# Kernel optimization log

Measured on AMD Instinct MI355X. Metric: run time of the kernel, lower is better.

The kernel has to match this reference:

```python
import jax, jax.numpy as jnp
import numpy as np

DIM = 512; LAYERS = 6; K = 15; VOCAB = 32000; B = 2; L = 1024
HID = 1024  # SwiGLU hidden: int(512*2) rounded up to multiple of 64
RANK = 64; BLOCK = 2048; MIX_W = 0.1
UP_DIL = [1, 2, 4, 8, 16, 32]
DN_DIL = UP_DIL[::-1]


def rmsnorm(x, w, eps=1e-6):
    return x * jax.lax.rsqrt(jnp.mean(x * x, axis=-1, keepdims=True) + eps) * w


def dconv(x, w, b, dil):
    # x: [B,D,T]; w: [D,1,K] depthwise; left (causal) padding of (K-1)*dil
    pad = (w.shape[-1] - 1) * dil
    y = jax.lax.conv_general_dilated(
        x, w, window_strides=(1,), padding=[(pad, 0)], rhs_dilation=(dil,),
        dimension_numbers=('NCH', 'OIH', 'NCH'), feature_group_count=x.shape[1])
    return y + b[None, :, None]


def conv_block(x, nw, cw, cb, w1, w2, w3, dil):
    # CausalDilatedConv: RMSNorm -> depthwise causal dilated conv -> silu -> SwiGLU -> +residual
    h = rmsnorm(x, nw)
    h = jax.nn.silu(dconv(jnp.transpose(h, (0, 2, 1)), cw, cb, dil))
    h = jnp.transpose(h, (0, 2, 1))
    h = jnp.einsum('bth,dh->btd',
                   jax.nn.silu(jnp.einsum('btd,hd->bth', h, w1)) * jnp.einsum('btd,hd->bth', h, w3),
                   w2)
    return h + x


def run_stack(x, dils, nw, cw, cb, w1, w2, w3, kp, ki, kd, gnorm):
    integral = x; previous = x; current = x
    for i, d in enumerate(dils):
        if i > 0:
            # PIDGate: step == i >= 1 so max(step,1) == i
            pid = kp[i-1] * current + ki[i-1] * (integral / i) + kd[i-1] * (current - previous)
            cur_in = rmsnorm(jax.nn.silu(pid), gnorm[i-1])
        else:
            cur_in = current
        current = conv_block(cur_in, nw[i], cw[i], cb[i], w1[i], w2[i], w3[i], d)
        previous = current
        integral = integral + current
    return current


def mix(x):
    # CausalMeanPool: x + 0.1 * causal running mean
    counts = jnp.arange(1, x.shape[1] + 1, dtype=x.dtype)[None, :, None]
    return x + MIX_W * jnp.cumsum(x, axis=1) / counts


def sgate(new, old, nw, dw, db, uw, ub):
    h = jax.nn.silu(rmsnorm(new, nw) @ dw.T + db)
    g = jax.nn.sigmoid(h @ uw.T + ub)
    return g * new + (1.0 - g) * old


def setup_inputs() -> dict:
    key = jax.random.key(0)
    ks = iter(jax.random.split(key, 64))
    def nrm(shape, s=0.02):
        return jax.random.normal(next(ks), shape, jnp.float32) * s
    def stack_params(p):
        return {
            p + '_norm_w': jnp.ones((LAYERS, DIM), jnp.float32),
            p + '_conv_w': nrm((LAYERS, DIM, 1, K), 0.1),
            p + '_conv_b': jnp.zeros((LAYERS, DIM), jnp.float32),
            p + '_w1': nrm((LAYERS, HID, DIM)),
            p + '_w2': nrm((LAYERS, DIM, HID)),
            p + '_w3': nrm((LAYERS, HID, DIM)),
            p + '_kp': jnp.full((LAYERS - 1, DIM), 0.5, jnp.float32),
            p + '_ki': jnp.full((LAYERS - 1, DIM), 0.3, jnp.float32),
            p + '_kd': jnp.full((LAYERS - 1, DIM), 0.2, jnp.float32),
            p + '_gnorm': jnp.ones((LAYERS - 1, DIM), jnp.float32),
        }
    inp = {
        'idx': jax.random.randint(next(ks), (B, L), 0, VOCAB),
        'emb': nrm((VOCAB, DIM)),
        'pos': nrm((1, BLOCK, DIM)),
        'emb_norm_w': jnp.ones((DIM,), jnp.float32),
        'token_shift': jnp.full((DIM,), 0.5, jnp.float32),
        'mem_gate_w': jnp.zeros((DIM, DIM), jnp.float32),  # nn.init.zeros_
        'mem_gate_b': nrm((DIM,)),
        'memory_p': jnp.zeros((B, DIM), jnp.float32),  # buffer, zero after reset()
        'sg_norm': jnp.ones((3, DIM), jnp.float32),
        'sg_down_w': nrm((3, RANK, DIM)),
        'sg_down_b': jnp.zeros((3, RANK), jnp.float32),
        'sg_up_w': nrm((3, DIM, RANK)),
        'sg_up_b': jnp.zeros((3, DIM), jnp.float32),
        'final_norm_w': jnp.ones((DIM,), jnp.float32),
    }
    inp.update(stack_params('up'))
    inp.update(stack_params('dn'))
    return inp


def _forward(idx, emb, pos, emb_norm_w, token_shift, mem_gate_w, mem_gate_b, memory_p,
             up_norm_w, up_conv_w, up_conv_b, up_w1, up_w2, up_w3, up_kp, up_ki, up_kd, up_gnorm,
             dn_norm_w, dn_conv_w, dn_conv_b, dn_w1, dn_w2, dn_w3, dn_kp, dn_ki, dn_kd, dn_gnorm,
             sg_norm, sg_down_w, sg_down_b, sg_up_w, sg_up_b, final_norm_w):
    T = idx.shape[1]
    x = emb[idx] + pos[:, :T]
    x = rmsnorm(x, emb_norm_w)
    # dropout is identity at eval time
    # memory injection: token-shift mix + sigmoid-gated persistent P-memory
    shifted = jnp.concatenate(
        [x[:, :1], token_shift * x[:, :-1] + (1.0 - token_shift) * x[:, 1:]], axis=1)
    mem = jax.nn.sigmoid(memory_p @ mem_gate_w.T + mem_gate_b)
    x = shifted + mem[:, None, :]
    initial = x
    up_p = (up_norm_w, up_conv_w, up_conv_b, up_w1, up_w2, up_w3, up_kp, up_ki, up_kd, up_gnorm)
    dn_p = (dn_norm_w, dn_conv_w, dn_conv_b, dn_w1, dn_w2, dn_w3, dn_kp, dn_ki, dn_kd, dn_gnorm)
    up1 = mix(run_stack(x, UP_DIL, *up_p))
    gated1 = sgate(up1, initial, sg_norm[0], sg_down_w[0], sg_down_b[0], sg_up_w[0], sg_up_b[0])
    down = mix(run_stack(gated1, DN_DIL, *dn_p))
    gated2 = sgate(down, initial, sg_norm[1], sg_down_w[1], sg_down_b[1], sg_up_w[1], sg_up_b[1])
    up2 = mix(run_stack(gated2, UP_DIL, *up_p))  # up_stack weights are shared/reused
    output = sgate(up2, gated2, sg_norm[2], sg_down_w[2], sg_down_b[2], sg_up_w[2], sg_up_b[2])
    output = rmsnorm(output, final_norm_w)
    return output @ emb.T  # tied head


def reference(idx, emb, pos, emb_norm_w, token_shift, mem_gate_w, mem_gate_b, memory_p,
              up_norm_w, up_conv_w, up_conv_b, up_w1, up_w2, up_w3, up_kp, up_ki, up_kd, up_gnorm,
              dn_norm_w, dn_conv_w, dn_conv_b, dn_w1, dn_w2, dn_w3, dn_kp, dn_ki, dn_kd, dn_gnorm,
              sg_norm, sg_down_w, sg_down_b, sg_up_w, sg_up_b, final_norm_w):
    return _forward(idx, emb, pos, emb_norm_w, token_shift, mem_gate_w, mem_gate_b, memory_p,
                    up_norm_w, up_conv_w, up_conv_b, up_w1, up_w2, up_w3, up_kp, up_ki, up_kd, up_gnorm,
                    dn_norm_w, dn_conv_w, dn_conv_b, dn_w1, dn_w2, dn_w3, dn_kp, dn_ki, dn_kd, dn_gnorm,
                    sg_norm, sg_down_w, sg_down_b, sg_up_w, sg_up_b, final_norm_w)
```

## Files before the change

kernel.cpp:

```cpp
#include <hip/hip_runtime.h>
#include <math.h>

#define DIM 512
#define NLAYERS 6
#define KSZ 15
#define VOCAB 32000
#define BATCH 2
#define SEQ 1024
#define HIDN 1024
#define RANK 64
#define NTOK (BATCH*SEQ)
#define MIXW 0.1f

typedef unsigned short u16;
typedef _Float16 f16;
typedef _Float16 f16x8 __attribute__((ext_vector_type(8)));
typedef _Float16 f16x4 __attribute__((ext_vector_type(4)));
typedef float  f32x4  __attribute__((ext_vector_type(4)));

__device__ __forceinline__ float sigm(float x){ return 1.f/(1.f+__expf(-x)); }

__device__ __forceinline__ float wred(float v){
  #pragma unroll
  for (int o=32;o>0;o>>=1) v += __shfl_xor(v, o, 64);
  return v;
}

#define MFMA16(a,b,c) __builtin_amdgcn_mfma_f32_16x16x32_f16(a,b,c,0,0,0)

__device__ __forceinline__ void gld16(const f16* g, f16* l){
  __builtin_amdgcn_global_load_lds(
      (const __attribute__((address_space(1))) void*)g,
      (__attribute__((address_space(3))) void*)l, 16, 0, 0);
}

template<int N> __device__ __forceinline__ void vwait(){
  asm volatile("s_waitcnt vmcnt(%0)" :: "i"(N) : "memory");
}
__device__ __forceinline__ void pipe_bar(){
  __builtin_amdgcn_s_barrier();
  __builtin_amdgcn_sched_barrier(0);
}

__global__ __launch_bounds__(256) void k_cvt(const float* __restrict__ s,
    f16* __restrict__ d, long n4){
  long i = (long)blockIdx.x*256 + threadIdx.x;
  if (i >= n4) return;
  float4 v = reinterpret_cast<const float4*>(s)[i];
  f16x4 o; o.x=(f16)v.x; o.y=(f16)v.y; o.z=(f16)v.z; o.w=(f16)v.w;
  reinterpret_cast<f16x4*>(d)[i] = o;
}

__global__ __launch_bounds__(256) void k_cvtconv(const float* __restrict__ cw,
    float* __restrict__ cwT, int n){
  int i = blockIdx.x*256 + threadIdx.x;
  if (i >= n) return;
  int d = i & (DIM-1); int m = (i >> 9) % KSZ; int l = i / (KSZ*DIM);
  cwT[i] = cw[((size_t)l*DIM + d)*KSZ + (KSZ-1-m)];
}

__global__ __launch_bounds__(64) void k_embnorm(const int* __restrict__ idx,
    const float* __restrict__ emb, const float* __restrict__ pos,
    const float* __restrict__ w, float* __restrict__ out){
  int row = blockIdx.x;
  int t = row & (SEQ-1);
  int lane = threadIdx.x;
  long ebase = (long)idx[row]*DIM;
  long pbase = (long)t*DIM;
  float v[8]; float ss = 0.f;
  #pragma unroll
  for (int c=0;c<2;c++){
    int d = c*256 + lane*4;
    float4 e = *reinterpret_cast<const float4*>(emb + ebase + d);
    float4 p = *reinterpret_cast<const float4*>(pos + pbase + d);
    float x0 = e.x+p.x, x1 = e.y+p.y, x2 = e.z+p.z, x3 = e.w+p.w;
    v[c*4+0]=x0; v[c*4+1]=x1; v[c*4+2]=x2; v[c*4+3]=x3;
    ss += x0*x0 + x1*x1 + x2*x2 + x3*x3;
  }
  ss = wred(ss);
  float rs = rsqrtf(ss*(1.f/DIM) + 1e-6f);
  long ob = (long)row*DIM;
  #pragma unroll
  for (int c=0;c<2;c++){
    int d = c*256 + lane*4;
    float4 wv = *reinterpret_cast<const float4*>(w + d);
    float4 o;
    o.x = v[c*4+0]*rs*wv.x; o.y = v[c*4+1]*rs*wv.y;
    o.z = v[c*4+2]*rs*wv.z; o.w = v[c*4+3]*rs*wv.w;
    *reinterpret_cast<float4*>(out + ob + d) = o;
  }
}

__global__ void k_mem(const float* __restrict__ p, const float* __restrict__ gw,
                      const float* __restrict__ gb, float* __restrict__ mem){
  int i = blockIdx.x*blockDim.x + threadIdx.x;
  if (i >= BATCH*DIM) return;
  int b = i >> 9, d = i & (DIM-1);
  float acc = gb[d];
  const float* wr = gw + (long)d*DIM;
  const float* pr = p + b*DIM;
  for (int k=0;k<DIM;k+=4){
    float4 wv = *reinterpret_cast<const float4*>(wr+k);
    float4 pv = *reinterpret_cast<const float4*>(pr+k);
    acc += wv.x*pv.x + wv.y*pv.y + wv.z*pv.z + wv.w*pv.w;
  }
  mem[i] = sigm(acc);
}

__global__ void k_shift(const float* __restrict__ xn, const float* __restrict__ mem,
    const float* __restrict__ ts, float* __restrict__ out){
  int i = blockIdx.x*256 + threadIdx.x;
  int d = i & (DIM-1); int row = i >> 9; int t = row & (SEQ-1); int b = row >> 10;
  float cur = xn[i];
  float v;
  if (t == 0) v = cur;
  else { float f = ts[d]; v = f*xn[i-DIM] + (1.f-f)*cur; }
  out[i] = v + mem[b*DIM + d];
}

__global__ __launch_bounds__(64) void k_rms(const float* __restrict__ x,
    const float* __restrict__ w, f16* __restrict__ oh){
  int row = blockIdx.x; int lane = threadIdx.x;
  const float* xr = x + (long)row*DIM;
  float v[8]; float ss = 0.f;
  #pragma unroll
  for (int c=0;c<2;c++){
    int d = c*256 + lane*4;
    float4 f = *reinterpret_cast<const float4*>(xr + d);
    v[c*4+0]=f.x; v[c*4+1]=f.y; v[c*4+2]=f.z; v[c*4+3]=f.w;
    ss += f.x*f.x + f.y*f.y + f.z*f.z + f.w*f.w;
  }
  ss = wred(ss);
  float rs = rsqrtf(ss*(1.f/DIM) + 1e-6f);
  long ob = (long)row*DIM;
  #pragma unroll
  for (int c=0;c<2;c++){
    int d = c*256 + lane*4;
    float4 wv = *reinterpret_cast<const float4*>(w + d);
    f16x4 o;
    o.x = (f16)(v[c*4+0]*rs*wv.x); o.y = (f16)(v[c*4+1]*rs*wv.y);
    o.z = (f16)(v[c*4+2]*rs*wv.z); o.w = (f16)(v[c*4+3]*rs*wv.w);
    *reinterpret_cast<f16x4*>(oh + ob + d) = o;
  }
}

__global__ __launch_bounds__(64) void k_pid(const float* __restrict__ C,
    const float* __restrict__ I, float inv_i,
    const float* __restrict__ kp, const float* __restrict__ ki,
    const float* __restrict__ gn, const float* __restrict__ nw,
    float* __restrict__ xin, f16* __restrict__ oh){
  int row = blockIdx.x; int lane = threadIdx.x;
  long base = (long)row*DIM;
  float u[8]; float ss = 0.f;
  #pragma unroll
  for (int c=0;c<2;c++){
    int d = c*256 + lane*4;
    float4 cv = *reinterpret_cast<const float4*>(C + base + d);
    float4 iv = *reinterpret_cast<const float4*>(I + base + d);
    float4 kpv = *reinterpret_cast<const float4*>(kp + d);
    float4 kiv = *reinterpret_cast<const float4*>(ki + d);
    float p0 = kpv.x*cv.x + kiv.x*(iv.x*inv_i);
    float p1 = kpv.y*cv.y + kiv.y*(iv.y*inv_i);
    float p2 = kpv.z*cv.z + kiv.z*(iv.z*inv_i);
    float p3 = kpv.w*cv.w + kiv.w*(iv.w*inv_i);
    float s0 = p0*sigm(p0), s1 = p1*sigm(p1), s2 = p2*sigm(p2), s3 = p3*sigm(p3);
    u[c*4+0]=s0; u[c*4+1]=s1; u[c*4+2]=s2; u[c*4+3]=s3;
    ss += s0*s0 + s1*s1 + s2*s2 + s3*s3;
  }
  ss = wred(ss);
  float rs1 = rsqrtf(ss*(1.f/DIM) + 1e-6f);
  float x2[8]; float ss2 = 0.f;
  #pragma unroll
  for (int c=0;c<2;c++){
    int d = c*256 + lane*4;
    float4 gv = *reinterpret_cast<const float4*>(gn + d);
    float y0 = u[c*4+0]*rs1*gv.x, y1 = u[c*4+1]*rs1*gv.y;
    float y2 = u[c*4+2]*rs1*gv.z, y3 = u[c*4+3]*rs1*gv.w;
    x2[c*4+0]=y0; x2[c*4+1]=y1; x2[c*4+2]=y2; x2[c*4+3]=y3;
    ss2 += y0*y0 + y1*y1 + y2*y2 + y3*y3;
    float4 o; o.x=y0; o.y=y1; o.z=y2; o.w=y3;
    *reinterpret_cast<float4*>(xin + base + d) = o;
  }
  ss2 = wred(ss2);
  float rs2 = rsqrtf(ss2*(1.f/DIM) + 1e-6f);
  #pragma unroll
  for (int c=0;c<2;c++){
    int d = c*256 + lane*4;
    float4 nv = *reinterpret_cast<const float4*>(nw + d);
    f16x4 o;
    o.x = (f16)(x2[c*4+0]*rs2*nv.x); o.y = (f16)(x2[c*4+1]*rs2*nv.y);
    o.z = (f16)(x2[c*4+2]*rs2*nv.z); o.w = (f16)(x2[c*4+3]*rs2*nv.w);
    *reinterpret_cast<f16x4*>(oh + base + d) = o;
  }
}

__global__ __launch_bounds__(256) void k_conv(const f16* __restrict__ h1,
    const float* __restrict__ cwT, const float* __restrict__ cb,
    f16* __restrict__ hc, int dil){
  int i = blockIdx.x*256 + threadIdx.x;
  int d8 = (i & 63) << 3; int row = i >> 6; int t = row & (SEQ-1);
  float acc[8];
  {
    float4 b0 = *reinterpret_cast<const float4*>(&cb[d8]);
    float4 b1 = *reinterpret_cast<const float4*>(&cb[d8+4]);
    acc[0]=b0.x; acc[1]=b0.y; acc[2]=b0.z; acc[3]=b0.w;
    acc[4]=b1.x; acc[5]=b1.y; acc[6]=b1.z; acc[7]=b1.w;
  }
  #pragma unroll
  for (int m=0;m<KSZ;m++){
    if (t - m*dil >= 0){
      f16x8 h = *reinterpret_cast<const f16x8*>(&h1[(size_t)(row - m*dil)*DIM + d8]);
      float4 w0 = *reinterpret_cast<const float4*>(&cwT[m*DIM + d8]);
      float4 w1 = *reinterpret_cast<const float4*>(&cwT[m*DIM + d8 + 4]);
      acc[0]+=w0.x*(float)h[0]; acc[1]+=w0.y*(float)h[1];
      acc[2]+=w0.z*(float)h[2]; acc[3]+=w0.w*(float)h[3];
      acc[4]+=w1.x*(float)h[4]; acc[5]+=w1.y*(float)h[5];
      acc[6]+=w1.z*(float)h[6]; acc[7]+=w1.w*(float)h[7];
    }
  }
  f16x8 o;
  #pragma unroll
  for (int j=0;j<8;j++){ o[j] = (f16)(acc[j]*sigm(acc[j])); }
  *reinterpret_cast<f16x8*>(&hc[(size_t)row*DIM + d8]) = o;
}


__global__ __launch_bounds__(256) void k_dual(const f16* __restrict__ A,
    const f16* __restrict__ W1, const f16* __restrict__ W3, f16* __restrict__ G){
  __shared__ __align__(16) f16 smem[4*8192];
  int tid = threadIdx.x, lane = tid&63, wid = tid>>6;
  int m0 = blockIdx.x*64, n0 = blockIdx.y*64;
  int r16 = lane&15, kq = lane>>4;

  f16x8 areg[8][2];
  {
    const f16* arow = A + (size_t)(m0 + wid*16 + r16)*512;
    #pragma unroll
    for (int t=0;t<8;t++)
      #pragma unroll
      for (int kk=0;kk<2;kk++)
        areg[t][kk] = *reinterpret_cast<const f16x8*>(arow + t*64 + (kk*4+kq)*8);
  }

  auto stage = [&](int buf, int t){
    #pragma unroll
    for (int j=0;j<4;j++){
      int cc = j*256 + tid;
      int mat = cc>>9, c2 = cc&511, r = c2>>3, s = c2&7;
      const f16* src = (mat ? W3 : W1) + (size_t)(n0+r)*512 + t*64 + ((s^(r&7))<<3);
      gld16(src, smem + buf*8192 + (j*256 + wid*64)*8);
    }
  };
  f32x4 a1[4] = {}, a3[4] = {};
#define DCOMP(T) { \
    const f16* sbt = smem + ((T)&3)*8192; \
    _Pragma("unroll") \
    for (int kk=0;kk<2;kk++){ \
      int kp0 = kk*4 + kq; \
      _Pragma("unroll") \
      for (int nf=0;nf<4;nf++){ \
        int row = nf*16 + r16; \
        f16x8 b1 = *reinterpret_cast<const f16x8*>(&sbt[row*64 + ((kp0^(row&7))<<3)]); \
        f16x8 b3 = *reinterpret_cast<const f16x8*>(&sbt[4096 + row*64 + ((kp0^(row&7))<<3)]); \
        a1[nf] = MFMA16(areg[T][kk], b1, a1[nf]); \
        a3[nf] = MFMA16(areg[T][kk], b3, a3[nf]); \
      } \
    } }
  stage(0,0); stage(1,1); stage(2,2);
#define DITER(T,NW) { vwait<NW>(); pipe_bar(); if ((T)+3 < 8) stage(((T)+3)&3,(T)+3); DCOMP(T); }
  DITER(0,8) DITER(1,8) DITER(2,8) DITER(3,8) DITER(4,8) DITER(5,8) DITER(6,4) DITER(7,0)
#undef DITER
#undef DCOMP
  __syncthreads();
  float* stg = (float*)smem + wid*1088;
  int dr = (lane>>4)*4, dc = lane&15;
  #pragma unroll
  for (int nf=0;nf<4;nf++)
    #pragma unroll
    for (int q=0;q<4;q++){
      float x1 = a1[nf][q];
      stg[(dr+q)*68 + nf*16 + dc] = x1*sigm(x1)*a3[nf][q];
    }
  int gmb = m0 + wid*16;
  #pragma unroll
  for (int pass=0;pass<2;pass++){
    int rr = pass*8 + (lane>>3), c = 8*(lane&7);
    float4 lo = *reinterpret_cast<float4*>(&stg[rr*68 + c]);
    float4 hi = *reinterpret_cast<float4*>(&stg[rr*68 + c + 4]);
    f16x8 o;
    o[0]=(f16)lo.x; o[1]=(f16)lo.y; o[2]=(f16)lo.z; o[3]=(f16)lo.w;
    o[4]=(f16)hi.x; o[5]=(f16)hi.y; o[6]=(f16)hi.z; o[7]=(f16)hi.w;
    *reinterpret_cast<f16x8*>(&G[(size_t)(gmb+rr)*HIDN + n0 + c]) = o;
  }
}

__global__ __launch_bounds__(256) void k_w2(const f16* __restrict__ A,
    const f16* __restrict__ W, const float* __restrict__ XIN,
    float* __restrict__ OF, float* __restrict__ I, int init){
  __shared__ __align__(16) f16 smem[4*4096];
  int tid = threadIdx.x, lane = tid&63, wid = tid>>6;
  int m0 = blockIdx.x*64, n0 = blockIdx.y*32;
  int r16 = lane&15, kq = lane>>4;

  f16x8 areg[8][4];
  {
    const f16* arow = A + (size_t)(m0 + wid*16 + r16)*1024;
    #pragma unroll
    for (int t=0;t<8;t++)
      #pragma unroll
      for (int kk=0;kk<4;kk++)
        areg[t][kk] = *reinterpret_cast<const f16x8*>(arow + t*128 + (kk*4+kq)*8);
  }

  auto stage = [&](int buf, int t){
    #pragma unroll
    for (int j=0;j<2;j++){
      int cc = j*256 + tid;
      int r = cc>>4, s = cc&15;
      int g = (s&8) | ((s^(r&7))&7);
      const f16* src = W + (size_t)(n0+r)*1024 + t*128 + (g<<3);
      gld16(src, smem + buf*4096 + (j*256 + wid*64)*8);
    }
  };
  f32x4 acc[2] = {};
#define WCOMP(T) { \
    const f16* sbt = smem + ((T)&3)*4096; \
    _Pragma("unroll") \
    for (int kk=0;kk<4;kk++){ \
      int kp0 = kk*4 + kq; \
      _Pragma("unroll") \
      for (int nf=0;nf<2;nf++){ \
        int row = nf*16 + r16; \
        int sl = (kp0&8) | ((kp0^(row&7))&7); \
        f16x8 bv = *reinterpret_cast<const f16x8*>(&sbt[row*128 + (sl<<3)]); \
        acc[nf] = MFMA16(areg[T][kk], bv, acc[nf]); \
      } \
    } }
  stage(0,0); stage(1,1); stage(2,2);
#define WITER(T,NW) { vwait<NW>(); pipe_bar(); if ((T)+3 < 8) stage(((T)+3)&3,(T)+3); WCOMP(T); }
  WITER(0,4) WITER(1,4) WITER(2,4) WITER(3,4) WITER(4,4) WITER(5,4) WITER(6,2) WITER(7,0)
#undef WITER
#undef WCOMP
  __syncthreads();
  float* stg = (float*)smem + wid*(16*36);
  int dr = (lane>>4)*4, dc = lane&15;
  #pragma unroll
  for (int nf=0;nf<2;nf++)
    #pragma unroll
    for (int q=0;q<4;q++)
      stg[(dr+q)*36 + nf*16 + dc] = acc[nf][q];
  int gmb = m0 + wid*16;
  #pragma unroll
  for (int pass=0;pass<2;pass++){
    int rr = pass*8 + (lane>>3), c = 4*(lane&7);
    float4 v = *reinterpret_cast<float4*>(&stg[rr*36 + c]);
    size_t o = (size_t)(gmb+rr)*DIM + n0 + c;
    float4 x = *reinterpret_cast<const float4*>(&XIN[o]);
    v.x+=x.x; v.y+=x.y; v.z+=x.z; v.w+=x.w;
    *reinterpret_cast<float4*>(&OF[o]) = v;
    float4 iv;
    if (init) iv = x;
    else      iv = *reinterpret_cast<const float4*>(&I[o]);
    iv.x+=v.x; iv.y+=v.y; iv.z+=v.z; iv.w+=v.w;
    *reinterpret_cast<float4*>(&I[o]) = iv;
  }
}

__global__ __launch_bounds__(512) void k_logits(const f16* __restrict__ A,
    const f16* __restrict__ E, float* __restrict__ OF){
  __shared__ __align__(16) char smemc[34816];
  f16* sB = (f16*)smemc;
  int tid = threadIdx.x, lane = tid&63, wid = tid>>6;
  int bid = blockIdx.x;
  int m0 = (bid&7)*256, n0 = (bid>>3)*64;
  int r16 = lane&15, kq = lane>>4;

  f16x8 areg[2][8][2];
  #pragma unroll
  for (int mf=0;mf<2;mf++){
    const f16* arow = A + (size_t)(m0 + wid*32 + mf*16 + r16)*512;
    #pragma unroll
    for (int t=0;t<8;t++)
      #pragma unroll
      for (int kk=0;kk<2;kk++)
        areg[mf][t][kk] = *reinterpret_cast<const f16x8*>(arow + t*64 + (kk*4+kq)*8);
  }

  auto stage = [&](int buf, int t){
    int cc = tid;
    int r = cc>>3, s = cc&7;
    gld16(E + (size_t)(n0+r)*512 + t*64 + ((s^(r&7))<<3), sB + buf*4096 + wid*64*8);
  };
  f32x4 acc[2][4] = {};
#define LCOMP(T) { \
    const f16* sbt = sB + ((T)&3)*4096; \
    _Pragma("unroll") \
    for (int kk=0;kk<2;kk++){ \
      int kp0 = kk*4 + kq; \
      _Pragma("unroll") \
      for (int nf=0;nf<4;nf++){ \
        int row = nf*16 + r16; \
        f16x8 bv = *reinterpret_cast<const f16x8*>(&sbt[row*64 + ((kp0^(row&7))<<3)]); \
        _Pragma("unroll") \
        for (int mf=0;mf<2;mf++) \
          acc[mf][nf] = MFMA16(areg[mf][T][kk], bv, acc[mf][nf]); \
      } \
    } }
  stage(0,0); stage(1,1); stage(2,2);
#define LITER(T,NW) { vwait<NW>(); pipe_bar(); if ((T)+3 < 8) stage(((T)+3)&3,(T)+3); LCOMP(T); }
  LITER(0,2) LITER(1,2) LITER(2,2) LITER(3,2) LITER(4,2) LITER(5,2) LITER(6,1) LITER(7,0)
#undef LITER
#undef LCOMP
  __syncthreads();
  int dr = (lane>>4)*4, dc = lane&15;
  float* stg = (float*)smemc + wid*1088;
  #pragma unroll
  for (int mf=0;mf<2;mf++){
    #pragma unroll
    for (int nf=0;nf<4;nf++)
      #pragma unroll
      for (int q=0;q<4;q++)
        stg[(dr+q)*68 + nf*16 + dc] = acc[mf][nf][q];
    int gmb = m0 + wid*32 + mf*16;
    #pragma unroll
    for (int pass=0;pass<4;pass++){
      int rr = pass*4 + (lane>>4), c = 4*(lane&15);
      float4 v = *reinterpret_cast<float4*>(&stg[rr*68 + c]);
      *reinterpret_cast<float4*>(&OF[(size_t)(gmb+rr)*VOCAB + n0 + c]) = v;
    }
  }
}

__global__ __launch_bounds__(64) void k_mix(float* __restrict__ x){
  int col = blockIdx.x;
  int b = col >> 9, d = col & (DIM-1);
  int lane = threadIdx.x;
  long o = (long)b*SEQ*DIM + d + (long)lane*16*DIM;
  float v[16]; float s = 0.f;
  #pragma unroll
  for (int j=0;j<16;j++){ v[j] = x[o + (long)j*DIM]; s += v[j]; }
  float t = s;
  #pragma unroll
  for (int off=1; off<64; off<<=1){
    float u = __shfl_up(t, off, 64);
    if (lane >= off) t += u;
  }
  float run = t - s;
  #pragma unroll
  for (int j=0;j<16;j++){
    run += v[j];
    int tt = lane*16 + j;
    x[o + (long)j*DIM] = v[j] + MIXW*run/(float)(tt+1);
  }
}

__global__ __launch_bounds__(256) void k_sgate(const float* __restrict__ xnew,
    const float* __restrict__ xold, const float* __restrict__ nw,
    const float* __restrict__ dw, const float* __restrict__ db,
    const float* __restrict__ uw, const float* __restrict__ ub,
    float* __restrict__ out){
  __shared__ float raw[DIM];
  __shared__ float xn[DIM];
  __shared__ float part[256];
  __shared__ float hb[RANK];
  int row = blockIdx.x, tid = threadIdx.x;
  long base = (long)row*DIM;
  float ss = 0.f;
  for (int d=tid; d<DIM; d+=256){ float v = xnew[base+d]; raw[d]=v; ss += v*v; }
  ss = wred(ss);
  if ((tid&63)==0) part[tid>>6] = ss;
  __syncthreads();
  float tot = part[0]+part[1]+part[2]+part[3];
  float rs = rsqrtf(tot*(1.f/DIM)+1e-6f);
  for (int d=tid; d<DIM; d+=256) xn[d] = raw[d]*rs*nw[d];
  __syncthreads();
  int rr = tid & 63, q = tid >> 6;
  float p = 0.f;
  const float* dwr = dw + (long)rr*DIM + q*128;
  const float* xq = xn + q*128;
  #pragma unroll 8
  for (int d=0; d<128; d+=4){
    float4 wv = *reinterpret_cast<const float4*>(dwr+d);
    p += xq[d]*wv.x + xq[d+1]*wv.y + xq[d+2]*wv.z + xq[d+3]*wv.w;
  }
  part[tid] = p;
  __syncthreads();
  if (tid < RANK){
    float h = part[tid] + part[64+tid] + part[128+tid] + part[192+tid] + db[tid];
    hb[tid] = h * sigm(h);
  }
  __syncthreads();
  for (int d=tid; d<DIM; d+=256){
    float a = ub[d];
    const float* ur = uw + (long)d*RANK;
    #pragma unroll
    for (int rj=0;rj<RANK;rj+=4){
      float4 uv = *reinterpret_cast<const float4*>(ur+rj);
      a += hb[rj]*uv.x + hb[rj+1]*uv.y + hb[rj+2]*uv.z + hb[rj+3]*uv.w;
    }
    float g = sigm(a);
    out[base+d] = g*raw[d] + (1.f-g)*xold[base+d];
  }
}

extern "C" void kernel_launch(void* const* d_in, const int* in_sizes, int n_in,
                              void* d_out, int out_size, void* d_ws, size_t ws_size,
                              hipStream_t stream){
  const int*   idx           = (const int*)d_in[0];
  const float* emb           = (const float*)d_in[1];
  const float* pos           = (const float*)d_in[2];
  const float* emb_norm_w    = (const float*)d_in[3];
  const float* token_shift   = (const float*)d_in[4];
  const float* mem_gate_w    = (const float*)d_in[5];
  const float* mem_gate_b    = (const float*)d_in[6];
  const float* memory_p      = (const float*)d_in[7];
  const float* sg_norm       = (const float*)d_in[8];
  const float* sg_down_w     = (const float*)d_in[9];
  const float* sg_down_b     = (const float*)d_in[10];
  const float* sg_up_w       = (const float*)d_in[11];
  const float* sg_up_b       = (const float*)d_in[12];
  const float* final_norm_w  = (const float*)d_in[13];
  struct StackP { const float *nw, *cw, *cb, *w1, *w2, *w3, *kp, *ki, *gn; };
  StackP up { (const float*)d_in[14], (const float*)d_in[15], (const float*)d_in[16],
              (const float*)d_in[17], (const float*)d_in[18], (const float*)d_in[19],
              (const float*)d_in[20], (const float*)d_in[21], (const float*)d_in[23] };
  StackP dn { (const float*)d_in[24], (const float*)d_in[25], (const float*)d_in[26],
              (const float*)d_in[27], (const float*)d_in[28], (const float*)d_in[29],
              (const float*)d_in[30], (const float*)d_in[31], (const float*)d_in[33] };

  char* wp = (char*)d_ws;
  auto alloc = [&](size_t bytes)->void*{
    void* p = (void*)wp; wp += (bytes + 255) & ~(size_t)255; return p;
  };
  float* A0  = (float*)alloc((size_t)NTOK*DIM*4);
  float* A1  = (float*)alloc((size_t)NTOK*DIM*4);
  float* Cb  = (float*)alloc((size_t)NTOK*DIM*4);
  float* Ib  = (float*)alloc((size_t)NTOK*DIM*4);
  float* XIN = (float*)alloc((size_t)NTOK*DIM*4);
  f16*   H1  = (f16*)alloc((size_t)NTOK*DIM*2);
  f16*   HC  = (f16*)alloc((size_t)NTOK*DIM*2);
  f16*   G   = (f16*)alloc((size_t)NTOK*HIDN*2);
  const size_t WSZ = (size_t)NLAYERS*HIDN*DIM;
  f16*   UpW1 = (f16*)alloc(WSZ*2);
  f16*   UpW2 = (f16*)alloc(WSZ*2);
  f16*   UpW3 = (f16*)alloc(WSZ*2);
  f16*   DnW1 = (f16*)alloc(WSZ*2);
  f16*   DnW2 = (f16*)alloc(WSZ*2);
  f16*   DnW3 = (f16*)alloc(WSZ*2);
  f16*   Ef   = (f16*)alloc((size_t)VOCAB*DIM*2);
  float* UpCT = (float*)alloc((size_t)NLAYERS*KSZ*DIM*4);
  float* DnCT = (float*)alloc((size_t)NLAYERS*KSZ*DIM*4);
  float* MEM  = (float*)alloc((size_t)BATCH*DIM*4);

  static const int updil[NLAYERS] = {1,2,4,8,16,32};
  static const int dndil[NLAYERS] = {32,16,8,4,2,1};

  {
    long n4 = WSZ/4;
    int g = (int)((n4 + 255)/256);
    k_cvt<<<g,256,0,stream>>>(up.w1, UpW1, n4);
    k_cvt<<<g,256,0,stream>>>(up.w2, UpW2, n4);
    k_cvt<<<g,256,0,stream>>>(up.w3, UpW3, n4);
    k_cvt<<<g,256,0,stream>>>(dn.w1, DnW1, n4);
    k_cvt<<<g,256,0,stream>>>(dn.w2, DnW2, n4);
    k_cvt<<<g,256,0,stream>>>(dn.w3, DnW3, n4);
    long e4 = (long)VOCAB*DIM/4;
    k_cvt<<<(int)((e4+255)/256),256,0,stream>>>(emb, Ef, e4);
    int nc = NLAYERS*KSZ*DIM;
    k_cvtconv<<<(nc+255)/256,256,0,stream>>>(up.cw, UpCT, nc);
    k_cvtconv<<<(nc+255)/256,256,0,stream>>>(dn.cw, DnCT, nc);
  }

  k_embnorm<<<NTOK,64,0,stream>>>(idx, emb, pos, emb_norm_w, Cb);
  k_mem<<<(BATCH*DIM+255)/256,256,0,stream>>>(memory_p, mem_gate_w, mem_gate_b, MEM);
  k_shift<<<NTOK*DIM/256,256,0,stream>>>(Cb, MEM, token_shift, A0);

  auto run_stack = [&](const float* xs, const StackP& S, const float* CT,
                       const f16* W1f, const f16* W2f, const f16* W3f, const int* dil){
    for (int l=0;l<NLAYERS;l++){
      const float* bin;
      if (l==0){
        bin = xs;
        k_rms<<<NTOK,64,0,stream>>>(xs, S.nw + l*DIM, H1);
      } else {
        k_pid<<<NTOK,64,0,stream>>>(Cb, Ib, 1.f/(float)l,
            S.kp+(l-1)*DIM, S.ki+(l-1)*DIM, S.gn+(l-1)*DIM, S.nw+l*DIM, XIN, H1);
        bin = XIN;
      }
      k_conv<<<NTOK*DIM/8/256,256,0,stream>>>(H1, CT + (size_t)l*KSZ*DIM, S.cb + l*DIM, HC, dil[l]);
      k_dual<<<dim3(NTOK/64, HIDN/64),256,0,stream>>>(
          HC, W1f + (size_t)l*HIDN*DIM, W3f + (size_t)l*HIDN*DIM, G);
      k_w2<<<dim3(NTOK/64, DIM/32),256,0,stream>>>(
          G, W2f + (size_t)l*DIM*HIDN, bin, Cb, Ib, (l==0)?1:0);
    }
  };

  run_stack(A0, up, UpCT, UpW1, UpW2, UpW3, updil);
  k_mix<<<BATCH*DIM,64,0,stream>>>(Cb);
  k_sgate<<<NTOK,256,0,stream>>>(Cb, A0, sg_norm, sg_down_w, sg_down_b, sg_up_w, sg_up_b, A1);
  run_stack(A1, dn, DnCT, DnW1, DnW2, DnW3, dndil);
  k_mix<<<BATCH*DIM,64,0,stream>>>(Cb);
  k_sgate<<<NTOK,256,0,stream>>>(Cb, A0, sg_norm+DIM, sg_down_w+RANK*DIM, sg_down_b+RANK,
                                 sg_up_w+DIM*RANK, sg_up_b+DIM, A1);
  run_stack(A1, up, UpCT, UpW1, UpW2, UpW3, updil);
  k_mix<<<BATCH*DIM,64,0,stream>>>(Cb);
  k_sgate<<<NTOK,256,0,stream>>>(Cb, A1, sg_norm+2*DIM, sg_down_w+2*RANK*DIM, sg_down_b+2*RANK,
                                 sg_up_w+2*DIM*RANK, sg_up_b+2*DIM, Cb);
  k_rms<<<NTOK,64,0,stream>>>(Cb, final_norm_w, H1);
  k_logits<<<8*(VOCAB/64),512,0,stream>>>(H1, Ef, (float*)d_out);
}
```

Baseline: 1.255 ms.

## Stream A-operand register loads through a 3-deep ring in GEMM kernels

The dual, w2 and logits GEMM kernels no longer load the whole A row tile into registers up front. A rows are now loaded per k-step into a 3-slot register ring, interleaved with the LDS staging of B, and the vmcnt wait counts are retuned to match the new number of outstanding loads. This cuts register pressure, which may raise occupancy, and avoids a long stall on the initial A load. The cost is more careful vmcnt accounting, where a wrong count would cause silent wrong results, plus extra sched barriers that constrain the compiler's instruction scheduling.

```diff
diff --git a/kernel.cpp b/kernel.cpp
--- a/kernel.cpp
+++ b/kernel.cpp
@@ -41,6 +41,7 @@
   __builtin_amdgcn_s_barrier();
   __builtin_amdgcn_sched_barrier(0);
 }
+#define SBAR() __builtin_amdgcn_sched_barrier(0)
 
 __global__ __launch_bounds__(256) void k_cvt(const float* __restrict__ s,
     f16* __restrict__ d, long n4){
@@ -231,16 +232,12 @@
   int tid = threadIdx.x, lane = tid&63, wid = tid>>6;
   int m0 = blockIdx.x*64, n0 = blockIdx.y*64;
   int r16 = lane&15, kq = lane>>4;
-
-  f16x8 areg[8][2];
-  {
-    const f16* arow = A + (size_t)(m0 + wid*16 + r16)*512;
-    #pragma unroll
-    for (int t=0;t<8;t++)
-      #pragma unroll
-      for (int kk=0;kk<2;kk++)
-        areg[t][kk] = *reinterpret_cast<const f16x8*>(arow + t*64 + (kk*4+kq)*8);
-  }
+  const f16* arow = A + (size_t)(m0 + wid*16 + r16)*512;
+
+  f16x8 areg[3][2];
+#define DALOAD(B,T) { \
+    areg[B][0] = *reinterpret_cast<const f16x8*>(arow + (T)*64 + (0*4+kq)*8); \
+    areg[B][1] = *reinterpret_cast<const f16x8*>(arow + (T)*64 + (1*4+kq)*8); }
 
   auto stage = [&](int buf, int t){
     #pragma unroll
@@ -262,15 +259,20 @@
         int row = nf*16 + r16; \
         f16x8 b1 = *reinterpret_cast<const f16x8*>(&sbt[row*64 + ((kp0^(row&7))<<3)]); \
         f16x8 b3 = *reinterpret_cast<const f16x8*>(&sbt[4096 + row*64 + ((kp0^(row&7))<<3)]); \
-        a1[nf] = MFMA16(areg[T][kk], b1, a1[nf]); \
-        a3[nf] = MFMA16(areg[T][kk], b3, a3[nf]); \
+        a1[nf] = MFMA16(areg[(T)%3][kk], b1, a1[nf]); \
+        a3[nf] = MFMA16(areg[(T)%3][kk], b3, a3[nf]); \
       } \
     } }
-  stage(0,0); stage(1,1); stage(2,2);
-#define DITER(T,NW) { vwait<NW>(); pipe_bar(); if ((T)+3 < 8) stage(((T)+3)&3,(T)+3); DCOMP(T); }
-  DITER(0,8) DITER(1,8) DITER(2,8) DITER(3,8) DITER(4,8) DITER(5,8) DITER(6,4) DITER(7,0)
+  DALOAD(0,0); DALOAD(1,1); SBAR();
+  stage(0,0); SBAR(); stage(1,1); SBAR(); stage(2,2);
+#define DITER(T,NW) { vwait<NW>(); pipe_bar(); \
+    if ((T)+2 < 8) DALOAD(((T)+2)%3, (T)+2); \
+    if ((T)+3 < 8) stage(((T)+3)&3, (T)+3); \
+    DCOMP(T); }
+  DITER(0,8) DITER(1,10) DITER(2,6) DITER(3,6) DITER(4,6) DITER(5,6) DITER(6,2) DITER(7,0)
 #undef DITER
 #undef DCOMP
+#undef DALOAD
   __syncthreads();
   float* stg = (float*)smem + wid*1088;
   int dr = (lane>>4)*4, dc = lane&15;
@@ -301,16 +303,14 @@
   int tid = threadIdx.x, lane = tid&63, wid = tid>>6;
   int m0 = blockIdx.x*64, n0 = blockIdx.y*32;
   int r16 = lane&15, kq = lane>>4;
-
-  f16x8 areg[8][4];
-  {
-    const f16* arow = A + (size_t)(m0 + wid*16 + r16)*1024;
-    #pragma unroll
-    for (int t=0;t<8;t++)
-      #pragma unroll
-      for (int kk=0;kk<4;kk++)
-        areg[t][kk] = *reinterpret_cast<const f16x8*>(arow + t*128 + (kk*4+kq)*8);
-  }
+  const f16* arow = A + (size_t)(m0 + wid*16 + r16)*1024;
+
+  f16x8 areg[3][4];
+#define WALOAD(B,T) { \
+    areg[B][0] = *reinterpret_cast<const f16x8*>(arow + (T)*128 + (0*4+kq)*8); \
+    areg[B][1] = *reinterpret_cast<const f16x8*>(arow + (T)*128 + (1*4+kq)*8); \
+    areg[B][2] = *reinterpret_cast<const f16x8*>(arow + (T)*128 + (2*4+kq)*8); \
+    areg[B][3] = *reinterpret_cast<const f16x8*>(arow + (T)*128 + (3*4+kq)*8); }
 
   auto stage = [&](int buf, int t){
     #pragma unroll
@@ -333,14 +333,19 @@
         int row = nf*16 + r16; \
         int sl = (kp0&8) | ((kp0^(row&7))&7); \
         f16x8 bv = *reinterpret_cast<const f16x8*>(&sbt[row*128 + (sl<<3)]); \
-        acc[nf] = MFMA16(areg[T][kk], bv, acc[nf]); \
+        acc[nf] = MFMA16(areg[(T)%3][kk], bv, acc[nf]); \
       } \
     } }
-  stage(0,0); stage(1,1); stage(2,2);
-#define WITER(T,NW) { vwait<NW>(); pipe_bar(); if ((T)+3 < 8) stage(((T)+3)&3,(T)+3); WCOMP(T); }
-  WITER(0,4) WITER(1,4) WITER(2,4) WITER(3,4) WITER(4,4) WITER(5,4) WITER(6,2) WITER(7,0)
+  WALOAD(0,0); WALOAD(1,1); SBAR();
+  stage(0,0); SBAR(); stage(1,1); SBAR(); stage(2,2);
+#define WITER(T,NW) { vwait<NW>(); pipe_bar(); \
+    if ((T)+2 < 8) WALOAD(((T)+2)%3, (T)+2); \
+    if ((T)+3 < 8) stage(((T)+3)&3, (T)+3); \
+    WCOMP(T); }
+  WITER(0,4) WITER(1,8) WITER(2,6) WITER(3,6) WITER(4,6) WITER(5,6) WITER(6,4) WITER(7,0)
 #undef WITER
 #undef WCOMP
+#undef WALOAD
   __syncthreads();
   float* stg = (float*)smem + wid*(16*36);
   int dr = (lane>>4)*4, dc = lane&15;
@@ -374,17 +379,15 @@
   int bid = blockIdx.x;
   int m0 = (bid&7)*256, n0 = (bid>>3)*64;
   int r16 = lane&15, kq = lane>>4;
-
-  f16x8 areg[2][8][2];
-  #pragma unroll
-  for (int mf=0;mf<2;mf++){
-    const f16* arow = A + (size_t)(m0 + wid*32 + mf*16 + r16)*512;
-    #pragma unroll
-    for (int t=0;t<8;t++)
-      #pragma unroll
-      for (int kk=0;kk<2;kk++)
-        areg[mf][t][kk] = *reinterpret_cast<const f16x8*>(arow + t*64 + (kk*4+kq)*8);
-  }
+  const f16* arow0 = A + (size_t)(m0 + wid*32 +      r16)*512;
+  const f16* arow1 = A + (size_t)(m0 + wid*32 + 16 + r16)*512;
+
+  f16x8 areg[3][2][2];
+#define LALOAD(B,T) { \
+    areg[B][0][0] = *reinterpret_cast<const f16x8*>(arow0 + (T)*64 + (0*4+kq)*8); \
+    areg[B][0][1] = *reinterpret_cast<const f16x8*>(arow0 + (T)*64 + (1*4+kq)*8); \
+    areg[B][1][0] = *reinterpret_cast<const f16x8*>(arow1 + (T)*64 + (0*4+kq)*8); \
+    areg[B][1][1] = *reinterpret_cast<const f16x8*>(arow1 + (T)*64 + (1*4+kq)*8); }
 
   auto stage = [&](int buf, int t){
     int cc = tid;
@@ -401,16 +404,20 @@
       for (int nf=0;nf<4;nf++){ \
         int row = nf*16 + r16; \
         f16x8 bv = *reinterpret_cast<const f16x8*>(&sbt[row*64 + ((kp0^(row&7))<<3)]); \
-        _Pragma("unroll") \
-        for (int mf=0;mf<2;mf++) \
-          acc[mf][nf] = MFMA16(areg[mf][T][kk], bv, acc[mf][nf]); \
+        acc[0][nf] = MFMA16(areg[(T)%3][0][kk], bv, acc[0][nf]); \
+        acc[1][nf] = MFMA16(areg[(T)%3][1][kk], bv, acc[1][nf]); \
       } \
     } }
-  stage(0,0); stage(1,1); stage(2,2);
-#define LITER(T,NW) { vwait<NW>(); pipe_bar(); if ((T)+3 < 8) stage(((T)+3)&3,(T)+3); LCOMP(T); }
-  LITER(0,2) LITER(1,2) LITER(2,2) LITER(3,2) LITER(4,2) LITER(5,2) LITER(6,1) LITER(7,0)
+  LALOAD(0,0); LALOAD(1,1); SBAR();
+  stage(0,0); SBAR(); stage(1,1); SBAR(); stage(2,2);
+#define LITER(T,NW) { vwait<NW>(); pipe_bar(); \
+    if ((T)+2 < 8) LALOAD(((T)+2)%3, (T)+2); \
+    if ((T)+3 < 8) stage(((T)+3)&3, (T)+3); \
+    LCOMP(T); }
+  LITER(0,2) LITER(1,6) LITER(2,5) LITER(3,5) LITER(4,5) LITER(5,5) LITER(6,4) LITER(7,0)
 #undef LITER
 #undef LCOMP
+#undef LALOAD
   __syncthreads();
   int dr = (lane>>4)*4, dc = lane&15;
   float* stg = (float*)smemc + wid*1088;
```

After: 1.126 ms. 1.11x faster.
